# Kernel optimization log

Measured on AMD Instinct MI355X. Metric: run time of the kernel, lower is better.

The kernel has to match this reference:

```python
import jax, jax.numpy as jnp
import numpy as np

DIM = 1024
AUX = 3
B, S = 32, 1024
ENC_D = DIM * AUX  # 3072


def setup_inputs() -> dict:
    key = jax.random.key(0)
    ks = jax.random.split(key, 5)
    sc1 = 1.0 / np.sqrt(DIM * (AUX + 1))
    sc3 = 1.0 / np.sqrt(ENC_D)
    return {
        "hidden_state": jax.random.normal(ks[0], (B, DIM), jnp.float32),
        "encoder_outputs": jax.random.normal(ks[1], (B, S, ENC_D), jnp.float32),
        "W1": jax.random.normal(ks[2], (DIM, DIM * (AUX + 1)), jnp.float32) * sc1,
        "b1": jnp.zeros((DIM,), jnp.float32),
        "w2": jax.random.normal(ks[3], (1, DIM), jnp.float32) * (1.0 / np.sqrt(DIM)),
        "W3": jax.random.normal(ks[4], (DIM, ENC_D), jnp.float32) * sc3,
        "b3": jnp.zeros((DIM,), jnp.float32),
    }


def reference(hidden_state, encoder_outputs, W1, b1, w2, W3, b3):
    # hidden_state: (B, dim); encoder_outputs: (B, S, dim*aux)
    Bsz, Slen, _ = encoder_outputs.shape
    h = jnp.broadcast_to(hidden_state[:, None, :], (Bsz, Slen, hidden_state.shape[-1]))
    inputs = jnp.concatenate([encoder_outputs, h], axis=2)  # (B, S, dim*(aux+1))
    # score MLP: tanh(linear1) -> linear2 (no bias)
    hidden = jnp.tanh(jnp.einsum('bsf,df->bsd', inputs, W1) + b1)  # (B, S, dim)
    e = jnp.einsum('bsd,od->bso', hidden, w2)[..., 0]  # (B, S)
    alpha = jax.nn.softmax(e, axis=1)
    context = jnp.einsum('bs,bsf->bf', alpha, encoder_outputs)  # (B, dim*aux)
    return jnp.einsum('bf,df->bd', context, W3) + b3  # (B, dim)
```

## Files before the change

### kernel.cpp

```cpp
#include <hip/hip_runtime.h>
#include <hip/hip_bf16.h>


typedef float          fx4 __attribute__((ext_vector_type(4)));
typedef short          sv8 __attribute__((ext_vector_type(8)));
typedef unsigned short uv4 __attribute__((ext_vector_type(4)));
typedef unsigned int   ui4 __attribute__((ext_vector_type(4)));

__device__ __forceinline__ unsigned short f2bf(float x) {
  unsigned u = __float_as_uint(x);
  return (unsigned short)((u + 0x7FFFu + ((u >> 16) & 1u)) >> 16);
}
__device__ __forceinline__ unsigned cvtpk(float lo, float hi) {
  unsigned r;
  asm("v_cvt_pk_bf16_f32 %0, %1, %2" : "=v"(r) : "v"(lo), "v"(hi));
  return r;
}
__device__ __forceinline__ ui4 pack8(fx4 a, fx4 b) {
  ui4 v;
  v[0] = cvtpk(a[0], a[1]); v[1] = cvtpk(a[2], a[3]);
  v[2] = cvtpk(b[0], b[1]); v[3] = cvtpk(b[2], b[3]);
  return v;
}

#define GLD(srcp, dstp)                                               \
  __builtin_amdgcn_global_load_lds(                                   \
      (const __attribute__((address_space(1))) void*)(srcp),          \
      (__attribute__((address_space(3))) void*)(dstp), 16, 0, 0)

__global__ void convw1_kernel(const float* __restrict__ W1, unsigned short* __restrict__ W1a) {
  int id = blockIdx.x * 256 + threadIdx.x;
  int d = id / 768, fi = id - d * 768;
  fx4 v = ((const fx4*)W1)[d * 1024 + fi];
  uv4 r; r[0] = f2bf(v[0]); r[1] = f2bf(v[1]); r[2] = f2bf(v[2]); r[3] = f2bf(v[3]);
  ((uv4*)W1a)[d * 768 + fi] = r;
}

__global__ void convenc_kernel(const float* __restrict__ enc, unsigned short* __restrict__ ebf) {
  int id = blockIdx.x * 256 + threadIdx.x;
  fx4 a = ((const fx4*)enc)[2 * id];
  fx4 b = ((const fx4*)enc)[2 * id + 1];
  ((ui4*)ebf)[id] = pack8(a, b);
}

__global__ void hbias_kernel(const float* __restrict__ hs, const float* __restrict__ W1,
                             const float* __restrict__ b1, float* __restrict__ hb) {
  int idx = (blockIdx.x << 2) + (threadIdx.x >> 6);
  int lane = threadIdx.x & 63;
  int b = idx >> 10, d = idx & 1023;
  const fx4* hv = (const fx4*)hs;
  const fx4* wv = (const fx4*)W1;
  float s = 0.f;
#pragma unroll
  for (int i = 0; i < 4; ++i) {
    int k4 = lane + (i << 6);
    fx4 h = hv[(b << 8) + k4];
    fx4 w = wv[d * 1024 + 768 + k4];
    s += h[0] * w[0] + h[1] * w[1] + h[2] * w[2] + h[3] * w[3];
  }
#pragma unroll
  for (int off = 32; off; off >>= 1) s += __shfl_xor(s, off);
  if (lane == 0) hb[idx] = s + b1[d];
}

__global__ __launch_bounds__(512, 2)
void gemm8(const unsigned short* __restrict__ Ag,
           const unsigned short* __restrict__ Bg,
           const float* __restrict__ hb,
           const float* __restrict__ w2,
           float* __restrict__ pe) {
  __shared__ __align__(16) unsigned short Ab[2][16384];

  const int t = threadIdx.x, lane = t & 63, wid = t >> 6;
  const int wm = wid >> 2, wn = wid & 3;

  const int bid = blockIdx.x;
  const int lg = ((bid & 7) << 6) | (bid >> 3);
  const int mt = lg >> 2, nt = lg & 3;
  const int row0 = mt << 8, col0 = nt << 8;

  const int l3 = lane >> 3, l7 = lane & 7;
  const unsigned short* asrc = Ag + (size_t)(row0 + wid * 32 + l3) * 3072 + ((l7 ^ l3) << 3);
  const int dstb = wid << 11;

  const int r15 = lane & 15, qv = lane >> 4;
  const int aB = (wm * 128 + r15) << 6;
  const int s0 = (qv ^ (r15 & 7)) << 3;
  const int s1 = ((qv + 4) ^ (r15 & 7)) << 3;

  const unsigned short* bp0 = Bg + (size_t)(col0 + wn * 64 + 0 * 16 + r15) * 3072 + qv * 8;
  const unsigned short* bp1 = Bg + (size_t)(col0 + wn * 64 + 1 * 16 + r15) * 3072 + qv * 8;
  const unsigned short* bp2 = Bg + (size_t)(col0 + wn * 64 + 2 * 16 + r15) * 3072 + qv * 8;
  const unsigned short* bp3 = Bg + (size_t)(col0 + wn * 64 + 3 * 16 + r15) * 3072 + qv * 8;

  fx4 acc[8][4] = {};
  sv8 bfv[2][8];

#define ST_A(AN, kt, g) GLD(asrc + (g) * 24576 + (kt) * 64, &Ab[AN][dstb + ((g) << 9)])
#define LDB(P, kh)                                                    \
  { bfv[P][(kh) * 4 + 0] = *(const sv8*)(bp0 + (kh) * 32);            \
    bfv[P][(kh) * 4 + 1] = *(const sv8*)(bp1 + (kh) * 32);            \
    bfv[P][(kh) * 4 + 2] = *(const sv8*)(bp2 + (kh) * 32);            \
    bfv[P][(kh) * 4 + 3] = *(const sv8*)(bp3 + (kh) * 32); }
#define BADV  { bp0 += 64; bp1 += 64; bp2 += 64; bp3 += 64; }

#define PHASE(P, MH, KH)                                              \
  { sv8 af[4];                                                        \
    const int sx = (KH) ? s1 : s0;                                    \
    _Pragma("unroll")                                                 \
    for (int mi = 0; mi < 4; ++mi)                                    \
      af[mi] = *(const sv8*)&Ab[P][aB + (((MH) * 64 + mi * 16) << 6) + sx]; \
    __builtin_amdgcn_s_setprio(1);                                    \
    _Pragma("unroll")                                                 \
    for (int mi = 0; mi < 4; ++mi)                                    \
      _Pragma("unroll")                                               \
      for (int ni = 0; ni < 4; ++ni)                                  \
        acc[(MH) * 4 + mi][ni] = __builtin_amdgcn_mfma_f32_16x16x32_bf16( \
            af[mi], bfv[P][(KH) * 4 + ni], acc[(MH) * 4 + mi][ni], 0, 0, 0); \
    __builtin_amdgcn_s_setprio(0);                                    \
  }

#define TILE(kt, P)                                                   \
  { if ((kt) < 47) { LDB(P ^ 1, 0) LDB(P ^ 1, 1) BADV                 \
                     ST_A(P ^ 1, (kt) + 1, 0); ST_A(P ^ 1, (kt) + 1, 1); \
                     ST_A(P ^ 1, (kt) + 1, 2); ST_A(P ^ 1, (kt) + 1, 3); } \
    PHASE(P, 0, 0)                                                    \
    PHASE(P, 1, 0)                                                    \
    PHASE(P, 0, 1)                                                    \
    PHASE(P, 1, 1)                                                    \
    asm volatile("s_waitcnt lgkmcnt(0)" ::: "memory");                \
    asm volatile("s_waitcnt vmcnt(0)" ::: "memory");                  \
    __builtin_amdgcn_s_barrier(); }

  ST_A(0, 0, 0); ST_A(0, 0, 1); ST_A(0, 0, 2); ST_A(0, 0, 3);
  LDB(0, 0) LDB(0, 1) BADV
  asm volatile("s_waitcnt vmcnt(0)" ::: "memory");
  __builtin_amdgcn_s_barrier();

  for (int it = 0; it < 24; ++it) {
    TILE(2 * it, 0)
    TILE(2 * it + 1, 1)
  }

  const int b = row0 >> 10;
  float w2v[4], hbv[4];
#pragma unroll
  for (int ni = 0; ni < 4; ++ni) {
    int c = col0 + wn * 64 + ni * 16 + r15;
    w2v[ni] = w2[c];
    hbv[ni] = hb[(b << 10) + c];
  }
#pragma unroll
  for (int mi = 0; mi < 8; ++mi) {
#pragma unroll
    for (int j = 0; j < 4; ++j) {
      float pz = 0.f;
#pragma unroll
      for (int ni = 0; ni < 4; ++ni)
        pz += tanhf(acc[mi][ni][j] + hbv[ni]) * w2v[ni];
      pz += __shfl_xor(pz, 1); pz += __shfl_xor(pz, 2);
      pz += __shfl_xor(pz, 4); pz += __shfl_xor(pz, 8);
      if (r15 == 0) {
        int row = row0 + wm * 128 + mi * 16 + (qv << 2) + j;
        pe[(row << 4) + (nt << 2) + wn] = pz;
      }
    }
  }
#undef ST_A
#undef LDB
#undef BADV
#undef PHASE
#undef TILE
}

__global__ __launch_bounds__(512, 2)
void gemm2(const float* __restrict__ enc,
           const unsigned short* __restrict__ W1a,
           const float* __restrict__ hb,
           const float* __restrict__ w2,
           float* __restrict__ pe) {
  __shared__ __align__(16) unsigned short As[2][10240];
  __shared__ __align__(16) unsigned short Bs[2][8192];
  const int t = threadIdx.x;
  const int lane = t & 63, wid = t >> 6;
  const int wm = wid >> 2, wn = wid & 3;
  const int bid = blockIdx.x;
  const int lg = ((bid & 7) << 6) | (bid >> 3);
  const int mt = lg >> 2, ntile = lg & 3;
  const int row0 = mt << 8;
  const int col0 = ntile << 8;
  const fx4* encv = (const fx4*)enc;
  const int ar = t >> 1, ah = t & 1;
  const int agb = (row0 + ar) * 768 + ah * 4;
  const int awb = ar * 40 + ah * 16;
  const int l3 = lane >> 3, l7 = lane & 7;
  const int pre = l7 ^ l3;
  const unsigned short* bsrc0 =
      W1a + (size_t)(col0 + wid * 32 + 2 * l3 + (pre >> 2)) * 3072 + (pre & 3) * 8;
  const unsigned short* bsrc1 = bsrc0 + (size_t)16 * 3072;
  const int bdst0 = (wid * 16) * 64;
  const int bdst1 = (wid * 16 + 8) * 64;
  const int r15 = lane & 15, qv = lane >> 4;
  const int aro = (wm * 128 + r15) * 40 + qv * 8;
  const int cb = wn * 64 + r15;
  const int bro = (cb >> 1) * 64 + (((((cb & 1) << 2) + qv) ^ ((cb >> 1) & 7)) << 3);
  fx4 acc[8][4] = {};
  fx4 pa[2][4];
#define A_LOAD(s, kt) { _Pragma("unroll") for (int j = 0; j < 4; ++j) pa[s][j] = encv[agb + (kt) * 8 + j]; }
#define A_WRITE(s, buf) { *(ui4*)&As[buf][awb] = pack8(pa[s][0], pa[s][1]); \
                          *(ui4*)&As[buf][awb + 8] = pack8(pa[s][2], pa[s][3]); }
#define B_ISSUE(buf, kt) { GLD(bsrc0 + (kt) * 32, &Bs[buf][bdst0]); \
                           GLD(bsrc1 + (kt) * 32, &Bs[buf][bdst1]); }
#define COMPUTE(p)                                                    \
  { sv8 af[8], bfv[4];                                                \
    _Pragma("unroll")                                                 \
    for (int mi = 0; mi < 8; ++mi) af[mi] = *(const sv8*)&As[p][aro + mi * 640]; \
    _Pragma("unroll")                                                 \
    for (int ni = 0; ni < 4; ++ni) bfv[ni] = *(const sv8*)&Bs[p][bro + ni * 512]; \
    _Pragma("unroll")                                                 \
    for (int mi = 0; mi < 8; ++mi)                                    \
      _Pragma("unroll")                                               \
      for (int ni = 0; ni < 4; ++ni)                                  \
        acc[mi][ni] = __builtin_amdgcn_mfma_f32_16x16x32_bf16(af[mi], bfv[ni], acc[mi][ni], 0, 0, 0); }
#define ITER(kt, p)                                                   \
  { COMPUTE(p)                                                        \
    if ((kt) < 95) { A_WRITE(p ^ 1, p ^ 1) }                          \
    if ((kt) < 93) { A_LOAD(p ^ 1, (kt) + 3) }                        \
    __builtin_amdgcn_s_barrier();                                     \
    if ((kt) < 94) {                                                  \
      B_ISSUE(p, (kt) + 2)                                            \
      asm volatile("s_waitcnt vmcnt(6)" ::: "memory");                \
    } else if ((kt) == 94) {                                          \
      asm volatile("s_waitcnt vmcnt(0)" ::: "memory");                \
    }                                                                 \
    asm volatile("s_waitcnt lgkmcnt(0)" ::: "memory");                \
    __builtin_amdgcn_s_barrier(); }
  A_LOAD(0, 0)
  A_LOAD(1, 1)
  B_ISSUE(0, 0)
  A_WRITE(0, 0)
  B_ISSUE(1, 1)
  A_LOAD(0, 2)
  asm volatile("s_waitcnt vmcnt(6)" ::: "memory");
  asm volatile("s_waitcnt lgkmcnt(0)" ::: "memory");
  __builtin_amdgcn_s_barrier();
  for (int kt2 = 0; kt2 < 48; ++kt2) {
    const int kt = kt2 * 2;
    ITER(kt, 0)
    ITER(kt + 1, 1)
  }
  const int b = row0 >> 10;
  float w2v[4], hbv[4];
#pragma unroll
  for (int ni = 0; ni < 4; ++ni) {
    int c = col0 + wn * 64 + ni * 16 + r15;
    w2v[ni] = w2[c];
    hbv[ni] = hb[(b << 10) + c];
  }
#pragma unroll
  for (int mi = 0; mi < 8; ++mi) {
#pragma unroll
    for (int j = 0; j < 4; ++j) {
      float pz = 0.f;
#pragma unroll
      for (int ni = 0; ni < 4; ++ni)
        pz += tanhf(acc[mi][ni][j] + hbv[ni]) * w2v[ni];
      pz += __shfl_xor(pz, 1); pz += __shfl_xor(pz, 2);
      pz += __shfl_xor(pz, 4); pz += __shfl_xor(pz, 8);
      if (r15 == 0) {
        int row = row0 + wm * 128 + mi * 16 + (qv << 2) + j;
        pe[(row << 4) + (ntile << 2) + wn] = pz;
      }
    }
  }
#undef A_LOAD
#undef A_WRITE
#undef B_ISSUE
#undef COMPUTE
#undef ITER
}

__global__ void softmax_kernel(const float* __restrict__ pe, float* __restrict__ alpha) {
  int b = blockIdx.x, t = threadIdx.x;
  int lane = t & 63, wid = t >> 6;
  float ev[4];
#pragma unroll
  for (int r = 0; r < 4; ++r) {
    int s = t + r * 256;
    const float* p = pe + ((b << 10) + s) * 16;
    float sum = 0.f;
#pragma unroll
    for (int i = 0; i < 16; ++i) sum += p[i];
    ev[r] = sum;
  }
  float m = fmaxf(fmaxf(ev[0], ev[1]), fmaxf(ev[2], ev[3]));
#pragma unroll
  for (int off = 32; off; off >>= 1) m = fmaxf(m, __shfl_xor(m, off));
  __shared__ float red[8];
  if (lane == 0) red[wid] = m;
  __syncthreads();
  m = fmaxf(fmaxf(red[0], red[1]), fmaxf(red[2], red[3]));
  float p4[4], ls = 0.f;
#pragma unroll
  for (int r = 0; r < 4; ++r) { p4[r] = expf(ev[r] - m); ls += p4[r]; }
#pragma unroll
  for (int off = 32; off; off >>= 1) ls += __shfl_xor(ls, off);
  if (lane == 0) red[4 + wid] = ls;
  __syncthreads();
  float inv = 1.0f / (red[4] + red[5] + red[6] + red[7]);
#pragma unroll
  for (int r = 0; r < 4; ++r) alpha[(b << 10) + t + r * 256] = p4[r] * inv;
}

__global__ void ctxpart_bf_kernel(const unsigned short* __restrict__ ebf,
                                  const float* __restrict__ alpha,
                                  float* __restrict__ part) {
  int bid = blockIdx.x, b = bid >> 4, sc = bid & 15;
  int t = threadIdx.x;
  __shared__ float sal[64];
  if (t < 64) sal[t] = alpha[(b << 10) + (sc << 6) + t];
  __syncthreads();
  const ui4* ev = (const ui4*)ebf;
  float a8[8] = {};
  int base = ((b << 10) + (sc << 6)) * 384;
  for (int si = 0; si < 64; ++si) {
    float a = sal[si];
    ui4 v = ev[base + si * 384 + t];
#pragma unroll
    for (int j = 0; j < 4; ++j) {
      unsigned u = v[j];
      a8[2 * j]     += a * __uint_as_float(u << 16);
      a8[2 * j + 1] += a * __uint_as_float(u & 0xFFFF0000u);
    }
  }
  fx4* pp = (fx4*)part;
  int pb = ((b << 4) + sc) * 768 + t * 2;
  fx4 o0 = {a8[0], a8[1], a8[2], a8[3]};
  fx4 o1 = {a8[4], a8[5], a8[6], a8[7]};
  pp[pb] = o0; pp[pb + 1] = o1;
}

__global__ void ctxpart_kernel(const float* __restrict__ enc, const float* __restrict__ alpha,
                               float* __restrict__ part) {
  int bid = blockIdx.x, b = bid >> 4, sc = bid & 15;
  int t = threadIdx.x;
  __shared__ float sal[64];
  if (t < 64) sal[t] = alpha[(b << 10) + (sc << 6) + t];
  __syncthreads();
  const fx4* ev = (const fx4*)enc;
  fx4 a0 = {}, a1 = {}, a2 = {};
  int base = ((b << 10) + (sc << 6)) * 768;
  for (int si = 0; si < 64; ++si) {
    float a = sal[si];
    const fx4* rp = ev + base + si * 768;
    a0 += a * rp[t];
    a1 += a * rp[256 + t];
    a2 += a * rp[512 + t];
  }
  fx4* pp = (fx4*)part;
  int pb = ((b << 4) + sc) * 768;
  pp[pb + t] = a0; pp[pb + 256 + t] = a1; pp[pb + 512 + t] = a2;
}

__global__ void ctxreduce_kernel(const float* __restrict__ part, float* __restrict__ ctx) {
  int j = blockIdx.x * 256 + threadIdx.x;
  int b = j / 768, fi = j - b * 768;
  const fx4* pp = (const fx4*)part;
  fx4 s = {};
#pragma unroll
  for (int i = 0; i < 16; ++i) s += pp[((b << 4) + i) * 768 + fi];
  ((fx4*)ctx)[b * 768 + fi] = s;
}

__global__ void final_kernel(const float* __restrict__ ctx, const float* __restrict__ W3,
                             const float* __restrict__ b3, float* __restrict__ out) {
  int idx = (blockIdx.x << 2) + (threadIdx.x >> 6);
  int lane = threadIdx.x & 63;
  int b = idx >> 10, d = idx & 1023;
  const fx4* cv = (const fx4*)ctx;
  const fx4* wv = (const fx4*)W3;
  float s = 0.f;
#pragma unroll
  for (int i = 0; i < 12; ++i) {
    int f4 = lane + (i << 6);
    fx4 c = cv[b * 768 + f4];
    fx4 w = wv[d * 768 + f4];
    s += c[0] * w[0] + c[1] * w[1] + c[2] * w[2] + c[3] * w[3];
  }
#pragma unroll
  for (int off = 32; off; off >>= 1) s += __shfl_xor(s, off);
  if (lane == 0) out[idx] = s + b3[d];
}

extern "C" void kernel_launch(void* const* d_in, const int* in_sizes, int n_in,
                              void* d_out, int out_size, void* d_ws, size_t ws_size,
                              hipStream_t stream) {
  const float* hs  = (const float*)d_in[0];
  const float* enc = (const float*)d_in[1];
  const float* W1  = (const float*)d_in[2];
  const float* b1  = (const float*)d_in[3];
  const float* w2  = (const float*)d_in[4];
  const float* W3  = (const float*)d_in[5];
  const float* b3  = (const float*)d_in[6];
  float* out = (float*)d_out;
  char* ws = (char*)d_ws;

  const size_t NEED_A = 216662016ULL;

  if (ws_size >= NEED_A) {
    unsigned short* ebf = (unsigned short*)(ws);
    unsigned short* W1a = (unsigned short*)(ws + 201326592);
    float* pe    = (float*)(ws + 207618048);
    float* alpha = (float*)(ws + 209715200);
    float* hb    = (float*)(ws + 209846272);
    float* ctx   = (float*)(ws + 209977344);
    float* part  = (float*)(ws + 210370560);

    convw1_kernel<<<3072, 256, 0, stream>>>(W1, W1a);
    convenc_kernel<<<49152, 256, 0, stream>>>(enc, ebf);
    hbias_kernel<<<8192, 256, 0, stream>>>(hs, W1, b1, hb);
    gemm8<<<512, 512, 0, stream>>>(ebf, W1a, hb, w2, pe);
    softmax_kernel<<<32, 256, 0, stream>>>(pe, alpha);
    ctxpart_bf_kernel<<<512, 384, 0, stream>>>(ebf, alpha, part);
    ctxreduce_kernel<<<96, 256, 0, stream>>>(part, ctx);
    final_kernel<<<8192, 256, 0, stream>>>(ctx, W3, b3, out);
  } else {
    unsigned short* W1a = (unsigned short*)(ws);
    float* pe    = (float*)(ws + 6291456);
    float* alpha = (float*)(ws + 8388608);
    float* hb    = (float*)(ws + 8519680);
    float* ctx   = (float*)(ws + 8650752);
    float* part  = (float*)(ws + 9043968);

    convw1_kernel<<<3072, 256, 0, stream>>>(W1, W1a);
    hbias_kernel<<<8192, 256, 0, stream>>>(hs, W1, b1, hb);
    gemm2<<<512, 512, 0, stream>>>(enc, W1a, hb, w2, pe);
    softmax_kernel<<<32, 256, 0, stream>>>(pe, alpha);
    ctxpart_kernel<<<512, 256, 0, stream>>>(enc, alpha, part);
    ctxreduce_kernel<<<96, 256, 0, stream>>>(part, ctx);
    final_kernel<<<8192, 256, 0, stream>>>(ctx, W3, b3, out);
  }
}
```

Before: 481.1 us.

## Shrink gemm8 tile to 128x128 and stage B through LDS

```diff
diff --git a/kernel.cpp b/kernel.cpp
--- a/kernel.cpp
+++ b/kernel.cpp
@@ -63,77 +63,73 @@
   if (lane == 0) hb[idx] = s + b1[d];
 }
 
-__global__ __launch_bounds__(512, 2)
+__global__ __launch_bounds__(256, 2)
 void gemm8(const unsigned short* __restrict__ Ag,
            const unsigned short* __restrict__ Bg,
            const float* __restrict__ hb,
            const float* __restrict__ w2,
            float* __restrict__ pe) {
-  __shared__ __align__(16) unsigned short Ab[2][16384];
+  __shared__ __align__(16) unsigned short Ab[2][8192];
+  __shared__ __align__(16) unsigned short Bb[2][8192];
 
   const int t = threadIdx.x, lane = t & 63, wid = t >> 6;
-  const int wm = wid >> 2, wn = wid & 3;
+  const int wm = wid >> 1, wn = wid & 1;
 
   const int bid = blockIdx.x;
-  const int lg = ((bid & 7) << 6) | (bid >> 3);
-  const int mt = lg >> 2, nt = lg & 3;
-  const int row0 = mt << 8, col0 = nt << 8;
+  const int lg = ((bid & 7) << 8) | (bid >> 3);
+  const int mt = lg >> 3, nt = lg & 7;
+  const int row0 = mt << 7, col0 = nt << 7;
 
   const int l3 = lane >> 3, l7 = lane & 7;
   const unsigned short* asrc = Ag + (size_t)(row0 + wid * 32 + l3) * 3072 + ((l7 ^ l3) << 3);
+  const unsigned short* bsrc = Bg + (size_t)(col0 + wid * 32 + l3) * 3072 + ((l7 ^ l3) << 3);
   const int dstb = wid << 11;
 
   const int r15 = lane & 15, qv = lane >> 4;
-  const int aB = (wm * 128 + r15) << 6;
+  const int aB = (wm * 64 + r15) << 6;
+  const int bB = (wn * 64 + r15) << 6;
   const int s0 = (qv ^ (r15 & 7)) << 3;
   const int s1 = ((qv + 4) ^ (r15 & 7)) << 3;
 
-  const unsigned short* bp0 = Bg + (size_t)(col0 + wn * 64 + 0 * 16 + r15) * 3072 + qv * 8;
-  const unsigned short* bp1 = Bg + (size_t)(col0 + wn * 64 + 1 * 16 + r15) * 3072 + qv * 8;
-  const unsigned short* bp2 = Bg + (size_t)(col0 + wn * 64 + 2 * 16 + r15) * 3072 + qv * 8;
-  const unsigned short* bp3 = Bg + (size_t)(col0 + wn * 64 + 3 * 16 + r15) * 3072 + qv * 8;
-
-  fx4 acc[8][4] = {};
-  sv8 bfv[2][8];
-
+  fx4 acc[4][4] = {};
+
+#define ST_B(BN, kt, g) GLD(bsrc + (g) * 24576 + (kt) * 64, &Bb[BN][dstb + ((g) << 9)])
 #define ST_A(AN, kt, g) GLD(asrc + (g) * 24576 + (kt) * 64, &Ab[AN][dstb + ((g) << 9)])
-#define LDB(P, kh)                                                    \
-  { bfv[P][(kh) * 4 + 0] = *(const sv8*)(bp0 + (kh) * 32);            \
-    bfv[P][(kh) * 4 + 1] = *(const sv8*)(bp1 + (kh) * 32);            \
-    bfv[P][(kh) * 4 + 2] = *(const sv8*)(bp2 + (kh) * 32);            \
-    bfv[P][(kh) * 4 + 3] = *(const sv8*)(bp3 + (kh) * 32); }
-#define BADV  { bp0 += 64; bp1 += 64; bp2 += 64; bp3 += 64; }
-
-#define PHASE(P, MH, KH)                                              \
-  { sv8 af[4];                                                        \
+
+#define PHASE(P, KH)                                                  \
+  { sv8 af[4], bfv[4];                                                \
     const int sx = (KH) ? s1 : s0;                                    \
     _Pragma("unroll")                                                 \
     for (int mi = 0; mi < 4; ++mi)                                    \
-      af[mi] = *(const sv8*)&Ab[P][aB + (((MH) * 64 + mi * 16) << 6) + sx]; \
+      af[mi] = *(const sv8*)&Ab[P][aB + (mi << 10) + sx];             \
+    _Pragma("unroll")                                                 \
+    for (int ni = 0; ni < 4; ++ni)                                    \
+      bfv[ni] = *(const sv8*)&Bb[P][bB + (ni << 10) + sx];            \
     __builtin_amdgcn_s_setprio(1);                                    \
     _Pragma("unroll")                                                 \
     for (int mi = 0; mi < 4; ++mi)                                    \
       _Pragma("unroll")                                               \
       for (int ni = 0; ni < 4; ++ni)                                  \
-        acc[(MH) * 4 + mi][ni] = __builtin_amdgcn_mfma_f32_16x16x32_bf16( \
-            af[mi], bfv[P][(KH) * 4 + ni], acc[(MH) * 4 + mi][ni], 0, 0, 0); \
+        acc[mi][ni] = __builtin_amdgcn_mfma_f32_16x16x32_bf16(        \
+            af[mi], bfv[ni], acc[mi][ni], 0, 0, 0);                   \
     __builtin_amdgcn_s_setprio(0);                                    \
   }
 
 #define TILE(kt, P)                                                   \
-  { if ((kt) < 47) { LDB(P ^ 1, 0) LDB(P ^ 1, 1) BADV                 \
-                     ST_A(P ^ 1, (kt) + 1, 0); ST_A(P ^ 1, (kt) + 1, 1); \
-                     ST_A(P ^ 1, (kt) + 1, 2); ST_A(P ^ 1, (kt) + 1, 3); } \
-    PHASE(P, 0, 0)                                                    \
-    PHASE(P, 1, 0)                                                    \
-    PHASE(P, 0, 1)                                                    \
-    PHASE(P, 1, 1)                                                    \
+  { if ((kt) < 47) {                                                  \
+      ST_B(P ^ 1, (kt) + 1, 0); ST_B(P ^ 1, (kt) + 1, 1);             \
+      ST_B(P ^ 1, (kt) + 1, 2); ST_B(P ^ 1, (kt) + 1, 3);             \
+      ST_A(P ^ 1, (kt) + 1, 0); ST_A(P ^ 1, (kt) + 1, 1);             \
+      ST_A(P ^ 1, (kt) + 1, 2); ST_A(P ^ 1, (kt) + 1, 3);             \
+    }                                                                 \
+    PHASE(P, 0)                                                       \
+    PHASE(P, 1)                                                       \
     asm volatile("s_waitcnt lgkmcnt(0)" ::: "memory");                \
     asm volatile("s_waitcnt vmcnt(0)" ::: "memory");                  \
     __builtin_amdgcn_s_barrier(); }
 
+  ST_B(0, 0, 0); ST_B(0, 0, 1); ST_B(0, 0, 2); ST_B(0, 0, 3);
   ST_A(0, 0, 0); ST_A(0, 0, 1); ST_A(0, 0, 2); ST_A(0, 0, 3);
-  LDB(0, 0) LDB(0, 1) BADV
   asm volatile("s_waitcnt vmcnt(0)" ::: "memory");
   __builtin_amdgcn_s_barrier();
 
@@ -151,7 +147,7 @@
     hbv[ni] = hb[(b << 10) + c];
   }
 #pragma unroll
-  for (int mi = 0; mi < 8; ++mi) {
+  for (int mi = 0; mi < 4; ++mi) {
 #pragma unroll
     for (int j = 0; j < 4; ++j) {
       float pz = 0.f;
@@ -161,14 +157,13 @@
       pz += __shfl_xor(pz, 1); pz += __shfl_xor(pz, 2);
       pz += __shfl_xor(pz, 4); pz += __shfl_xor(pz, 8);
       if (r15 == 0) {
-        int row = row0 + wm * 128 + mi * 16 + (qv << 2) + j;
-        pe[(row << 4) + (nt << 2) + wn] = pz;
+        int row = row0 + wm * 64 + mi * 16 + (qv << 2) + j;
+        pe[(row << 4) + (nt << 1) + wn] = pz;
       }
     }
   }
 #undef ST_A
-#undef LDB
-#undef BADV
+#undef ST_B
 #undef PHASE
 #undef TILE
 }
@@ -419,7 +414,7 @@
     convw1_kernel<<<3072, 256, 0, stream>>>(W1, W1a);
     convenc_kernel<<<49152, 256, 0, stream>>>(enc, ebf);
     hbias_kernel<<<8192, 256, 0, stream>>>(hs, W1, b1, hb);
-    gemm8<<<512, 512, 0, stream>>>(ebf, W1a, hb, w2, pe);
+    gemm8<<<2048, 256, 0, stream>>>(ebf, W1a, hb, w2, pe);
     softmax_kernel<<<32, 256, 0, stream>>>(pe, alpha);
     ctxpart_bf_kernel<<<512, 384, 0, stream>>>(ebf, alpha, part);
     ctxreduce_kernel<<<96, 256, 0, stream>>>(part, ctx);
```

Result: faster. 451.1 us (-6.2%).
